# Optimization experiments

Measured on AMD Instinct MI355X. Metric: run time of the kernel, lower is better.

The kernel has to match this reference:

```python
import jax, jax.numpy as jnp
import numpy as np
import math

D = 256       # d_model
H = 8         # n_head
HD = D // H   # head dim = 32
L = 24        # n_layer
DFF = 1024    # d_ff
MAX_STEP = 512
EPS = 1e-5


def _make_pe():
    # positions repeated in groups of 3 (repeat_integers)
    pos = np.repeat(np.arange(MAX_STEP), 3).astype(np.float32)[:, None]      # [3*MAX_STEP, 1]
    div = np.exp(np.arange(0, D, 2, dtype=np.float32) * (-math.log(10000.0) / D))[None, :]
    arg = pos @ div                                                          # [3*MAX_STEP, D/2]
    pe = np.zeros((MAX_STEP * 3, D), dtype=np.float32)
    pe[:, 0::2] = np.sin(arg)
    pe[:, 1::2] = np.cos(arg)
    return jnp.asarray(pe)


def setup_inputs() -> dict:
    key = jax.random.key(0)
    ks = jax.random.split(key, 14)
    B, S = 4, 1536
    s = 0.02
    f32 = jnp.float32
    inp = {
        "x": jax.random.normal(ks[0], (B, S, D), f32),
        "pe": _make_pe(),
        "Wqkv": jax.random.normal(ks[1], (L, 3 * D, D), f32) * s,
        "bqkv": jax.random.normal(ks[2], (L, 3 * D), f32) * s,
        "Wo": jax.random.normal(ks[3], (L, D, D), f32) * s,
        "bo": jax.random.normal(ks[4], (L, D), f32) * s,
        "W1": jax.random.normal(ks[5], (L, DFF, D), f32) * s,
        "b1": jax.random.normal(ks[6], (L, DFF), f32) * s,
        "W2": jax.random.normal(ks[7], (L, D, DFF), f32) * s,
        "b2": jax.random.normal(ks[8], (L, D), f32) * s,
        "ln1_g": jnp.ones((L, D), f32),
        "ln1_b": jnp.zeros((L, D), f32),
        "ln2_g": jnp.ones((L, D), f32),
        "ln2_b": jnp.zeros((L, D), f32),
    }
    return inp


def _layernorm(y, g, b):
    m = jnp.mean(y, axis=-1, keepdims=True)
    v = jnp.mean(jnp.square(y - m), axis=-1, keepdims=True)
    return (y - m) * jax.lax.rsqrt(v + EPS) * g + b


def reference(x, pe, Wqkv, bqkv, Wo, bo, W1, b1, W2, b2, ln1_g, ln1_b, ln2_g, ln2_b):
    B, S, Dm = x.shape
    # positional embedding (positions shared within groups of 3)
    h = x + pe[None, :S]
    # block-causal mask: token i (step i//3) may attend to keys j with j//3 <= i//3
    steps = jnp.arange(S) // 3
    mask = jnp.where(steps[None, :] <= steps[:, None], 0.0, -jnp.inf)  # [S, S]
    scale = 1.0 / math.sqrt(HD)

    def layer(h, p):
        wqkv, bq, wo, bo_, w1, b1_, w2, b2_, g1, be1, g2, be2 = p
        qkv = h @ wqkv.T + bq                       # [B,S,3D]
        q, k, v = jnp.split(qkv, 3, axis=-1)
        q = q.reshape(B, S, H, HD)
        k = k.reshape(B, S, H, HD)
        v = v.reshape(B, S, H, HD)
        scores = jnp.einsum('bqhd,bkhd->bhqk', q, k) * scale + mask
        attn = jax.nn.softmax(scores, axis=-1)
        o = jnp.einsum('bhqk,bkhd->bqhd', attn, v).reshape(B, S, Dm)
        o = o @ wo.T + bo_
        h = _layernorm(h + o, g1, be1)              # post-LN
        f = jax.nn.gelu(h @ w1.T + b1_, approximate=False) @ w2.T + b2_
        h = _layernorm(h + f, g2, be2)
        return h, None

    params = (Wqkv, bqkv, Wo, bo, W1, b1, W2, b2, ln1_g, ln1_b, ln2_g, ln2_b)
    out, _ = jax.lax.scan(layer, h, params)
    return out
```

## Files before the change

kernel.cpp:

```cpp
#include <hip/hip_runtime.h>
#include <math.h>

#define SEQ   1536
#define BATCH 4
#define ROWS  (BATCH*SEQ)
#define DM    256
#define NH    8
#define HDIM  32
#define NL    24
#define DFFN  1024

typedef __bf16  bf16x4 __attribute__((ext_vector_type(4)));
typedef __bf16  bf16x8 __attribute__((ext_vector_type(8)));
typedef float   f32x4  __attribute__((ext_vector_type(4)));

__device__ __forceinline__ unsigned short f2bf(float f) {
    union { float f; unsigned int u; } v; v.f = f;
    return (unsigned short)((v.u + 0x7fffu + ((v.u >> 16) & 1u)) >> 16);
}
__device__ __forceinline__ float bf2f(unsigned short u) {
    union { unsigned int i; float f; } v; v.i = ((unsigned int)u) << 16; return v.f;
}

__device__ __forceinline__ void gload16(const void* g, void* l) {
    __builtin_amdgcn_global_load_lds(
        (const __attribute__((address_space(1))) void*)g,
        (__attribute__((address_space(3))) void*)l, 16, 0, 0);
}

__global__ __launch_bounds__(256) void w2bf_kernel(
    const float* __restrict__ src, unsigned short* __restrict__ dst)
{
    int i = (blockIdx.x * 256 + threadIdx.x) * 8;
    float4 a = *(const float4*)(src + i);
    float4 b = *(const float4*)(src + i + 4);
    union { unsigned short u[8]; uint4 v; } pk;
    pk.u[0] = f2bf(a.x); pk.u[1] = f2bf(a.y); pk.u[2] = f2bf(a.z); pk.u[3] = f2bf(a.w);
    pk.u[4] = f2bf(b.x); pk.u[5] = f2bf(b.y); pk.u[6] = f2bf(b.z); pk.u[7] = f2bf(b.w);
    *(uint4*)(dst + i) = pk.v;
}

__global__ __launch_bounds__(256) void pe_add_kernel(
    const float* __restrict__ x, const float* __restrict__ pe,
    float* __restrict__ h, unsigned short* __restrict__ hb)
{
    int i4  = blockIdx.x * 256 + threadIdx.x;
    int idx = i4 * 4;
    int row = idx >> 8;
    int d   = idx & 255;
    int s   = row % SEQ;
    float4 xv = *(const float4*)(x + idx);
    float4 pv = *(const float4*)(pe + s * DM + d);
    float4 hv;
    hv.x = xv.x + pv.x; hv.y = xv.y + pv.y; hv.z = xv.z + pv.z; hv.w = xv.w + pv.w;
    *(float4*)(h + idx) = hv;
    ushort4 hbv;
    hbv.x = f2bf(hv.x); hbv.y = f2bf(hv.y); hbv.z = f2bf(hv.z); hbv.w = f2bf(hv.w);
    *(ushort4*)(hb + idx) = hbv;
}

template<int K, int EPI>
__global__ __launch_bounds__(256) void gemm3(
    const unsigned short* __restrict__ A,
    const unsigned short* __restrict__ W,
    const float* __restrict__ bias,
    unsigned short* __restrict__ outb,
    unsigned short* __restrict__ vT)
{
    __shared__ unsigned short Ash[2][128 * 64];
    __shared__ unsigned short Bsh[2][64 * 64];
    const int m0 = blockIdx.x * 128;
    const int n0 = blockIdx.y * 64;
    const int t  = threadIdx.x;
    const int lane = t & 63;
    const int wv = t >> 6;
    const int wm = wv >> 1, wn = wv & 1;
    const int l15 = lane & 15, l4 = lane >> 4;

    const int ar = lane >> 3;
    const int sx = ((lane & 7) ^ ar) * 8;

    f32x4 acc[4][2];
    #pragma unroll
    for (int i = 0; i < 4; ++i) { acc[i][0] = (f32x4){0,0,0,0}; acc[i][1] = (f32x4){0,0,0,0}; }

    const int NT = K / 64;
    #pragma unroll
    for (int i = 0; i < 4; ++i) {
        int c = wv * 4 + i;
        gload16(&A[(size_t)(m0 + c * 8 + ar) * K + sx], &Ash[0][c * 512]);
    }
    gload16(&W[(size_t)(n0 + wv * 8 + ar) * K + sx],        &Bsh[0][wv * 512]);
    gload16(&W[(size_t)(n0 + (wv + 4) * 8 + ar) * K + sx],  &Bsh[0][(wv + 4) * 512]);
    __syncthreads();

    int cur = 0;
    for (int tt = 0; tt < NT; ++tt) {
        if (tt + 1 < NT) {
            const int k0 = (tt + 1) * 64;
            #pragma unroll
            for (int i = 0; i < 4; ++i) {
                int c = wv * 4 + i;
                gload16(&A[(size_t)(m0 + c * 8 + ar) * K + k0 + sx], &Ash[cur ^ 1][c * 512]);
            }
            gload16(&W[(size_t)(n0 + wv * 8 + ar) * K + k0 + sx],       &Bsh[cur ^ 1][wv * 512]);
            gload16(&W[(size_t)(n0 + (wv + 4) * 8 + ar) * K + k0 + sx], &Bsh[cur ^ 1][(wv + 4) * 512]);
        }
        #pragma unroll
        for (int kk = 0; kk < 2; ++kk) {
            bf16x8 af[4], bfr[2];
            #pragma unroll
            for (int mt = 0; mt < 4; ++mt) {
                int row = wm * 64 + mt * 16 + l15;
                af[mt] = *(const bf16x8*)&Ash[cur][row * 64 + (((kk * 4 + l4) ^ (l15 & 7)) * 8)];
            }
            #pragma unroll
            for (int nt = 0; nt < 2; ++nt) {
                int row = wn * 32 + nt * 16 + l15;
                bfr[nt] = *(const bf16x8*)&Bsh[cur][row * 64 + (((kk * 4 + l4) ^ (l15 & 7)) * 8)];
            }
            #pragma unroll
            for (int mt = 0; mt < 4; ++mt)
                #pragma unroll
                for (int nt = 0; nt < 2; ++nt)
                    acc[mt][nt] = __builtin_amdgcn_mfma_f32_16x16x32_bf16(af[mt], bfr[nt], acc[mt][nt], 0, 0, 0);
        }
        __syncthreads();
        cur ^= 1;
    }

    #pragma unroll
    for (int mt = 0; mt < 4; ++mt)
    #pragma unroll
    for (int nt = 0; nt < 2; ++nt)
    #pragma unroll
    for (int r = 0; r < 4; ++r) {
        int row = m0 + wm * 64 + mt * 16 + l4 * 4 + r;
        int col = n0 + wn * 32 + nt * 16 + l15;
        float val = acc[mt][nt][r] + bias[col];
        if (EPI == 0) {
            if (col < 512) {
                if (col < 256) val *= 0.17677669529663687f;
                outb[(size_t)row * 512 + col] = f2bf(val);
            } else {
                int c = col - 512; int hh = c >> 5; int d = c & 31;
                int b = row / SEQ; int s = row - b * SEQ;
                vT[(((size_t)(b * NH + hh)) * HDIM + d) * SEQ + s] = f2bf(val);
            }
        } else {
            float g = 0.5f * val * (1.0f + erff(val * 0.70710678118654752f));
            outb[(size_t)row * DFFN + col] = f2bf(g);
        }
    }
}

template<int K>
__global__ __launch_bounds__(256) void gemm_ln(
    const unsigned short* __restrict__ A,
    const unsigned short* __restrict__ W,
    const float* __restrict__ bias,
    const float* __restrict__ resid,
    const float* __restrict__ gam, const float* __restrict__ bet,
    float* __restrict__ hout, unsigned short* __restrict__ hbout)
{
    __shared__ unsigned short Ash[2][32 * 64];
    __shared__ unsigned short Bsh[2][256 * 64];
    __shared__ float red[4][32][2];
    const int m0 = blockIdx.x * 32;
    const int t  = threadIdx.x;
    const int lane = t & 63;
    const int w  = t >> 6;
    const int l15 = lane & 15, l4 = lane >> 4;
    const int ar = lane >> 3;
    const int sx = ((lane & 7) ^ ar) * 8;

    f32x4 acc[2][4];
    #pragma unroll
    for (int mt = 0; mt < 2; ++mt)
        #pragma unroll
        for (int nt = 0; nt < 4; ++nt)
            acc[mt][nt] = (f32x4){0,0,0,0};

    const int NT = K / 64;
    gload16(&A[(size_t)(m0 + w * 8 + ar) * K + sx], &Ash[0][w * 512]);
    #pragma unroll
    for (int i = 0; i < 8; ++i) {
        int c = w * 8 + i;
        gload16(&W[(size_t)(c * 8 + ar) * K + sx], &Bsh[0][c * 512]);
    }
    __syncthreads();

    int cur = 0;
    for (int tt = 0; tt < NT; ++tt) {
        if (tt + 1 < NT) {
            const int k0 = (tt + 1) * 64;
            gload16(&A[(size_t)(m0 + w * 8 + ar) * K + k0 + sx], &Ash[cur ^ 1][w * 512]);
            #pragma unroll
            for (int i = 0; i < 8; ++i) {
                int c = w * 8 + i;
                gload16(&W[(size_t)(c * 8 + ar) * K + k0 + sx], &Bsh[cur ^ 1][c * 512]);
            }
        }
        #pragma unroll
        for (int kk = 0; kk < 2; ++kk) {
            bf16x8 af[2], bfr[4];
            #pragma unroll
            for (int mt = 0; mt < 2; ++mt) {
                int row = mt * 16 + l15;
                af[mt] = *(const bf16x8*)&Ash[cur][row * 64 + (((kk * 4 + l4) ^ (l15 & 7)) * 8)];
            }
            #pragma unroll
            for (int nt = 0; nt < 4; ++nt) {
                int row = w * 64 + nt * 16 + l15;
                bfr[nt] = *(const bf16x8*)&Bsh[cur][row * 64 + (((kk * 4 + l4) ^ (l15 & 7)) * 8)];
            }
            #pragma unroll
            for (int mt = 0; mt < 2; ++mt)
                #pragma unroll
                for (int nt = 0; nt < 4; ++nt)
                    acc[mt][nt] = __builtin_amdgcn_mfma_f32_16x16x32_bf16(af[mt], bfr[nt], acc[mt][nt], 0, 0, 0);
        }
        __syncthreads();
        cur ^= 1;
    }

    float vals[2][4][4];
    float gc[4], bc[4];
    #pragma unroll
    for (int nt = 0; nt < 4; ++nt) {
        int col = w * 64 + nt * 16 + l15;
        gc[nt] = gam[col];
        bc[nt] = bet[col];
    }
    #pragma unroll
    for (int mt = 0; mt < 2; ++mt)
        #pragma unroll
        for (int r = 0; r < 4; ++r) {
            int rowl = mt * 16 + l4 * 4 + r;
            float s = 0.f, s2 = 0.f;
            #pragma unroll
            for (int nt = 0; nt < 4; ++nt) {
                int col = w * 64 + nt * 16 + l15;
                float v = acc[mt][nt][r] + bias[col]
                        + resid[(size_t)(m0 + rowl) * DM + col];
                vals[mt][nt][r] = v;
                s += v; s2 += v * v;
            }
            s  += __shfl_xor(s, 1);  s2 += __shfl_xor(s2, 1);
            s  += __shfl_xor(s, 2);  s2 += __shfl_xor(s2, 2);
            s  += __shfl_xor(s, 4);  s2 += __shfl_xor(s2, 4);
            s  += __shfl_xor(s, 8);  s2 += __shfl_xor(s2, 8);
            if (l15 == 0) { red[w][rowl][0] = s; red[w][rowl][1] = s2; }
        }
    __syncthreads();

    #pragma unroll
    for (int mt = 0; mt < 2; ++mt)
        #pragma unroll
        for (int r = 0; r < 4; ++r) {
            int rowl = mt * 16 + l4 * 4 + r;
            float tot  = red[0][rowl][0] + red[1][rowl][0] + red[2][rowl][0] + red[3][rowl][0];
            float tot2 = red[0][rowl][1] + red[1][rowl][1] + red[2][rowl][1] + red[3][rowl][1];
            float mean = tot * (1.0f / 256.0f);
            float var  = tot2 * (1.0f / 256.0f) - mean * mean;
            float rstd = rsqrtf(var + 1e-5f);
            size_t base = (size_t)(m0 + rowl) * DM;
            #pragma unroll
            for (int nt = 0; nt < 4; ++nt) {
                int col = w * 64 + nt * 16 + l15;
                float y = (vals[mt][nt][r] - mean) * rstd * gc[nt] + bc[nt];
                hout[base + col]  = y;
                hbout[base + col] = f2bf(y);
            }
        }
}

template<int K, int EPI>
__global__ __launch_bounds__(256) void gemm2f(
    const unsigned short* __restrict__ A,
    const float* __restrict__ W,
    const float* __restrict__ bias,
    float* __restrict__ outf,
    unsigned short* __restrict__ outb,
    unsigned short* __restrict__ vT,
    const float* __restrict__ resid)
{
    __shared__ unsigned short Ash[64 * 64];
    __shared__ unsigned short Bsh[64 * 64];
    const int m0 = blockIdx.x * 64;
    const int n0 = blockIdx.y * 64;
    const int t  = threadIdx.x;
    const int lane = t & 63;
    const int wv = t >> 6;
    const int wm = wv >> 1, wn = wv & 1;
    const int l15 = lane & 15, l4 = lane >> 4;
    const int ar = lane >> 3;
    const int ac = (lane & 7) * 8;
    const int c0 = wv, c1 = wv + 4;

    f32x4 acc[2][2];
    #pragma unroll
    for (int i = 0; i < 2; ++i) { acc[i][0] = (f32x4){0,0,0,0}; acc[i][1] = (f32x4){0,0,0,0}; }

    for (int k0 = 0; k0 < K; k0 += 64) {
        gload16(&A[(size_t)(m0 + c0 * 8 + ar) * K + k0 + ac], &Ash[c0 * 512]);
        gload16(&A[(size_t)(m0 + c1 * 8 + ar) * K + k0 + ac], &Ash[c1 * 512]);
        {
            int row = t >> 2, seg = (t & 3) * 16;
            const float* gw = W + (size_t)(n0 + row) * K + k0 + seg;
            float4 w0 = *(const float4*)(gw);
            float4 w1 = *(const float4*)(gw + 4);
            float4 w2 = *(const float4*)(gw + 8);
            float4 w3 = *(const float4*)(gw + 12);
            union { unsigned short u[8]; uint4 v; } p0, p1;
            p0.u[0] = f2bf(w0.x); p0.u[1] = f2bf(w0.y); p0.u[2] = f2bf(w0.z); p0.u[3] = f2bf(w0.w);
            p0.u[4] = f2bf(w1.x); p0.u[5] = f2bf(w1.y); p0.u[6] = f2bf(w1.z); p0.u[7] = f2bf(w1.w);
            p1.u[0] = f2bf(w2.x); p1.u[1] = f2bf(w2.y); p1.u[2] = f2bf(w2.z); p1.u[3] = f2bf(w2.w);
            p1.u[4] = f2bf(w3.x); p1.u[5] = f2bf(w3.y); p1.u[6] = f2bf(w3.z); p1.u[7] = f2bf(w3.w);
            *(uint4*)&Bsh[row * 64 + seg] = p0.v;
            *(uint4*)&Bsh[row * 64 + seg + 8] = p1.v;
        }
        __syncthreads();
        #pragma unroll
        for (int kk = 0; kk < 2; ++kk) {
            bf16x8 af[2], bfr[2];
            #pragma unroll
            for (int mt = 0; mt < 2; ++mt)
                af[mt] = *(const bf16x8*)&Ash[(wm * 32 + mt * 16 + l15) * 64 + kk * 32 + l4 * 8];
            #pragma unroll
            for (int nt = 0; nt < 2; ++nt)
                bfr[nt] = *(const bf16x8*)&Bsh[(wn * 32 + nt * 16 + l15) * 64 + kk * 32 + l4 * 8];
            #pragma unroll
            for (int mt = 0; mt < 2; ++mt)
                #pragma unroll
                for (int nt = 0; nt < 2; ++nt)
                    acc[mt][nt] = __builtin_amdgcn_mfma_f32_16x16x32_bf16(af[mt], bfr[nt], acc[mt][nt], 0, 0, 0);
        }
        __syncthreads();
    }

    #pragma unroll
    for (int mt = 0; mt < 2; ++mt)
    #pragma unroll
    for (int nt = 0; nt < 2; ++nt)
    #pragma unroll
    for (int r = 0; r < 4; ++r) {
        int row = m0 + wm * 32 + mt * 16 + l4 * 4 + r;
        int col = n0 + wn * 32 + nt * 16 + l15;
        float val = acc[mt][nt][r] + bias[col];
        if (EPI == 0) {
            if (col < 512) {
                if (col < 256) val *= 0.17677669529663687f;
                outb[(size_t)row * 512 + col] = f2bf(val);
            } else {
                int c = col - 512; int hh = c >> 5; int d = c & 31;
                int b = row / SEQ; int s = row - b * SEQ;
                vT[(((size_t)(b * NH + hh)) * HDIM + d) * SEQ + s] = f2bf(val);
            }
        } else if (EPI == 1) {
            outf[(size_t)row * DM + col] = val + resid[(size_t)row * DM + col];
        } else {
            float g = 0.5f * val * (1.0f + erff(val * 0.70710678118654752f));
            outb[(size_t)row * DFFN + col] = f2bf(g);
        }
    }
}

__global__ __launch_bounds__(192) void attn6(
    const unsigned short* __restrict__ qkv,
    const unsigned short* __restrict__ vT,
    unsigned short* __restrict__ ob)
{
    const int sp   = threadIdx.x >> 6;
    const int lane = threadIdx.x & 63;
    const int qt = 47 - (int)blockIdx.x;
    const int bh = blockIdx.y;
    const int b = bh >> 3, h = bh & 7;
    const int l15 = lane & 15, l4 = lane >> 4;
    const int q0 = qt * 32;

    __shared__ unsigned short P[3][2][32 * 64];
    __shared__ float sml[3][96];

    const int kend   = ((q0 + 31) / 3) * 3 + 3;
    const int ntiles = (kend + 63) >> 6;
    const int t0 = (ntiles * sp) / 3;
    const int t1 = (ntiles * (sp + 1)) / 3;
    const bool empty = (t0 >= t1);

    float* Osp = (float*)P[sp];

    if (empty) {
        #pragma unroll
        for (int i = 0; i < 16; ++i) Osp[lane + i * 64] = 0.f;
        if (lane < 32) { sml[sp][lane] = 0.f; sml[sp][32 + lane] = 0.f; }
    } else {
        const int kendc = min(t1 * 64, kend);
        const int lim_min = (q0 / 3) * 3 + 3;

        bf16x8 qf[2];
        #pragma unroll
        for (int mt = 0; mt < 2; ++mt)
            qf[mt] = *(const bf16x8*)&qkv[((size_t)(b * SEQ + q0 + mt * 16 + l15)) * 512 + h * 32 + l4 * 8];

        const int sw = (l15 & 7) << 3;
        int lim2[2];
        lim2[0] = ((q0 + l15) / 3) * 3 + 3;
        lim2[1] = ((q0 + 16 + l15) / 3) * 3 + 3;

        float lsum[2] = {0.f, 0.f};
        f32x4 of[2][2];
        const f32x4 zf = (f32x4){0.f, 0.f, 0.f, 0.f};
        of[0][0] = zf; of[0][1] = zf; of[1][0] = zf; of[1][1] = zf;

        bf16x8 kf[4];
        #pragma unroll
        for (int kt = 0; kt < 4; ++kt)
            kf[kt] = *(const bf16x8*)&qkv[((size_t)(b * SEQ + t0 * 64 + kt * 16 + l15)) * 512 + 256 + h * 32 + l4 * 8];

        int pb = 0;
        for (int j0 = t0 * 64; j0 < kendc; j0 += 64) {
            f32x4 sf[2][4];
            #pragma unroll
            for (int mt = 0; mt < 2; ++mt)
                #pragma unroll
                for (int kt = 0; kt < 4; ++kt)
                    sf[mt][kt] = __builtin_amdgcn_mfma_f32_16x16x32_bf16(kf[kt], qf[mt], zf, 0, 0, 0);

            const int jn = (j0 + 64 < kendc) ? j0 + 64 : j0;
            bf16x8 kfn[4];
            #pragma unroll
            for (int kt = 0; kt < 4; ++kt)
                kfn[kt] = *(const bf16x8*)&qkv[((size_t)(b * SEQ + jn + kt * 16 + l15)) * 512 + 256 + h * 32 + l4 * 8];
            bf16x8 vf[2][2];
            #pragma unroll
            for (int dh = 0; dh < 2; ++dh)
                #pragma unroll
                for (int ks = 0; ks < 2; ++ks)
                    vf[dh][ks] = *(const bf16x8*)&vT[(((size_t)(b * NH + h)) * HDIM + dh * 16 + l15) * SEQ + j0 + ks * 32 + l4 * 8];

            const bool masked = (j0 + 64 > lim_min);
            #pragma unroll
            for (int mt = 0; mt < 2; ++mt) {
                const int rowq = mt * 16 + l15;
                float ls = 0.f;
                #pragma unroll
                for (int kt = 0; kt < 4; ++kt) {
                    float s0 = sf[mt][kt][0], s1 = sf[mt][kt][1];
                    float s2 = sf[mt][kt][2], s3 = sf[mt][kt][3];
                    if (masked) {
                        const int kb = j0 + kt * 16 + l4 * 4;
                        const int L = lim2[mt];
                        s0 = (kb     < L) ? s0 : -INFINITY;
                        s1 = (kb + 1 < L) ? s1 : -INFINITY;
                        s2 = (kb + 2 < L) ? s2 : -INFINITY;
                        s3 = (kb + 3 < L) ? s3 : -INFINITY;
                    }
                    float p0 = __expf(s0), p1 = __expf(s1);
                    float p2 = __expf(s2), p3 = __expf(s3);
                    ls += (p0 + p1) + (p2 + p3);
                    bf16x4 pk;
                    pk[0] = (__bf16)p0; pk[1] = (__bf16)p1;
                    pk[2] = (__bf16)p2; pk[3] = (__bf16)p3;
                    *(bf16x4*)&P[sp][pb][rowq * 64 + ((kt * 16 + l4 * 4) ^ sw)] = pk;
                }
                lsum[mt] += ls;
            }

            bf16x8 pf[2][2];
            #pragma unroll
            for (int mt = 0; mt < 2; ++mt) {
                int row = mt * 16 + l15;
                #pragma unroll
                for (int ks = 0; ks < 2; ++ks)
                    pf[mt][ks] = *(const bf16x8*)&P[sp][pb][row * 64 + ((ks * 32 + l4 * 8) ^ sw)];
            }
            #pragma unroll
            for (int mt = 0; mt < 2; ++mt)
                #pragma unroll
                for (int dh = 0; dh < 2; ++dh) {
                    of[mt][dh] = __builtin_amdgcn_mfma_f32_16x16x32_bf16(pf[mt][0], vf[dh][0], of[mt][dh], 0, 0, 0);
                    of[mt][dh] = __builtin_amdgcn_mfma_f32_16x16x32_bf16(pf[mt][1], vf[dh][1], of[mt][dh], 0, 0, 0);
                }
            #pragma unroll
            for (int kt = 0; kt < 4; ++kt) kf[kt] = kfn[kt];
            pb ^= 1;
        }

        int bad = (lsum[0] > 1.0e30f || lsum[1] > 1.0e30f) ? 1 : 0;
        if (__any(bad)) {
            int lim[2][4];
            float mrow[2][4], lsumO[2][4];
            #pragma unroll
            for (int mt = 0; mt < 2; ++mt) {
                of[mt][0] = zf; of[mt][1] = zf;
                #pragma unroll
                for (int r = 0; r < 4; ++r) {
                    mrow[mt][r] = -INFINITY; lsumO[mt][r] = 0.f;
                    int q = q0 + mt * 16 + l4 * 4 + r;
                    lim[mt][r] = (q / 3) * 3 + 3;
                }
            }
            for (int j0 = t0 * 64; j0 < kendc; j0 += 64) {
                bf16x8 kfs[4];
                #pragma unroll
                for (int kt = 0; kt < 4; ++kt)
                    kfs[kt] = *(const bf16x8*)&qkv[((size_t)(b * SEQ + j0 + kt * 16 + l15)) * 512 + 256 + h * 32 + l4 * 8];
                f32x4 sf[2][4];
                #pragma unroll
                for (int mt = 0; mt < 2; ++mt)
                    #pragma unroll
                    for (int kt = 0; kt < 4; ++kt)
                        sf[mt][kt] = __builtin_amdgcn_mfma_f32_16x16x32_bf16(qf[mt], kfs[kt], zf, 0, 0, 0);
                #pragma unroll
                for (int mt = 0; mt < 2; ++mt) {
                    float alpha[4];
                    #pragma unroll
                    for (int r = 0; r < 4; ++r) {
                        const int L = lim[mt][r]; int jb = j0 + l15;
                        float s0 = (jb      < L) ? sf[mt][0][r] : -INFINITY;
                        float s1 = (jb + 16 < L) ? sf[mt][1][r] : -INFINITY;
                        float s2 = (jb + 32 < L) ? sf[mt][2][r] : -INFINITY;
                        float s3 = (jb + 48 < L) ? sf[mt][3][r] : -INFINITY;
                        float tm = fmaxf(fmaxf(s0, s1), fmaxf(s2, s3));
                        tm = fmaxf(tm, __shfl_xor(tm, 1));
                        tm = fmaxf(tm, __shfl_xor(tm, 2));
                        tm = fmaxf(tm, __shfl_xor(tm, 4));
                        tm = fmaxf(tm, __shfl_xor(tm, 8));
                        float mn = fmaxf(mrow[mt][r], tm);
                        float a  = __expf(mrow[mt][r] - mn);
                        mrow[mt][r] = mn;
                        float p0 = __expf(s0 - mn), p1 = __expf(s1 - mn);
                        float p2 = __expf(s2 - mn), p3 = __expf(s3 - mn);
                        int row = mt * 16 + l4 * 4 + r;
                        int swo = (row & 7) << 3;
                        P[sp][1][(row * 64 +      l15) ^ swo] = f2bf(p0);
                        P[sp][1][(row * 64 + 16 + l15) ^ swo] = f2bf(p1);
                        P[sp][1][(row * 64 + 32 + l15) ^ swo] = f2bf(p2);
                        P[sp][1][(row * 64 + 48 + l15) ^ swo] = f2bf(p3);
                        lsumO[mt][r] = lsumO[mt][r] * a + (p0 + p1) + (p2 + p3);
                        alpha[r] = a;
                    }
                    f32x4 av = (f32x4){alpha[0], alpha[1], alpha[2], alpha[3]};
                    of[mt][0] *= av; of[mt][1] *= av;
                }
                bf16x8 pf[2][2], vf[2][2];
                #pragma unroll
                for (int mt = 0; mt < 2; ++mt) {
                    int row = mt * 16 + l15;
                    int swo = (row & 7) << 3;
                    #pragma unroll
                    for (int ks = 0; ks < 2; ++ks)
                        pf[mt][ks] = *(const bf16x8*)&P[sp][1][(row * 64 + ks * 32 + l4 * 8) ^ swo];
                }
                #pragma unroll
                for (int dh = 0; dh < 2; ++dh)
                    #pragma unroll
                    for (int ks = 0; ks < 2; ++ks)
                        vf[dh][ks] = *(const bf16x8*)&vT[(((size_t)(b * NH + h)) * HDIM + dh * 16 + l15) * SEQ + j0 + ks * 32 + l4 * 8];
                #pragma unroll
                for (int mt = 0; mt < 2; ++mt)
                    #pragma unroll
                    for (int dh = 0; dh < 2; ++dh) {
                        of[mt][dh] = __builtin_amdgcn_mfma_f32_16x16x32_bf16(pf[mt][0], vf[dh][0], of[mt][dh], 0, 0, 0);
                        of[mt][dh] = __builtin_amdgcn_mfma_f32_16x16x32_bf16(pf[mt][1], vf[dh][1], of[mt][dh], 0, 0, 0);
                    }
            }
            #pragma unroll
            for (int mt = 0; mt < 2; ++mt)
                #pragma unroll
                for (int r = 0; r < 4; ++r) {
                    float s = lsumO[mt][r];
                    s += __shfl_xor(s, 1);
                    s += __shfl_xor(s, 2);
                    s += __shfl_xor(s, 4);
                    s += __shfl_xor(s, 8);
                    lsumO[mt][r] = s;
                }
            #pragma unroll
            for (int mt = 0; mt < 2; ++mt)
                #pragma unroll
                for (int dh = 0; dh < 2; ++dh)
                    #pragma unroll
                    for (int r = 0; r < 4; ++r)
                        Osp[(mt * 16 + l4 * 4 + r) * 32 + dh * 16 + l15] = of[mt][dh][r];
            if (l15 == 0) {
                #pragma unroll
                for (int mt = 0; mt < 2; ++mt)
                    #pragma unroll
                    for (int r = 0; r < 4; ++r) {
                        int row = mt * 16 + l4 * 4 + r;
                        sml[sp][row]      = mrow[mt][r];
                        sml[sp][32 + row] = lsumO[mt][r];
                    }
            }
        } else {
            #pragma unroll
            for (int mt = 0; mt < 2; ++mt) {
                float s = lsum[mt];
                s += __shfl_xor(s, 16);
                s += __shfl_xor(s, 32);
                lsum[mt] = s;
            }
            #pragma unroll
            for (int mt = 0; mt < 2; ++mt)
                #pragma unroll
                for (int dh = 0; dh < 2; ++dh)
                    #pragma unroll
                    for (int r = 0; r < 4; ++r)
                        Osp[(mt * 16 + l4 * 4 + r) * 32 + dh * 16 + l15] = of[mt][dh][r];
            if (lane < 32) sml[sp][lane] = 0.f;
            if (l4 == 0) {
                sml[sp][32 + l15]      = lsum[0];
                sml[sp][32 + 16 + l15] = lsum[1];
            }
        }
    }

    __syncthreads();

    const int t = threadIdx.x;
    if (t < 128) {
        const int row = t >> 2;
        const int seg = (t & 3) * 8;
        float m0 = sml[0][row], l0 = sml[0][32 + row];
        float m1 = sml[1][row], l1 = sml[1][32 + row];
        float m2 = sml[2][row], l2 = sml[2][32 + row];
        float mt = fmaxf(fmaxf(m0, m1), m2);
        float w0 = __expf(m0 - mt), w1 = __expf(m1 - mt), w2 = __expf(m2 - mt);
        float inv = 1.0f / (w0 * l0 + w1 * l1 + w2 * l2);
        const float* O0 = (const float*)P[0];
        const float* O1 = (const float*)P[1];
        const float* O2 = (const float*)P[2];
        union { unsigned short u[8]; uint4 v; } pk;
        #pragma unroll
        for (int j = 0; j < 8; ++j) {
            int idx = row * 32 + seg + j;
            pk.u[j] = f2bf((w0 * O0[idx] + w1 * O1[idx] + w2 * O2[idx]) * inv);
        }
        *(uint4*)&ob[((size_t)(b * SEQ + q0 + row)) * DM + h * 32 + seg] = pk.v;
    }
}

__global__ __launch_bounds__(256) void ln_kernel(
    const float* __restrict__ rin,
    const float* __restrict__ gam, const float* __restrict__ bet,
    float* __restrict__ hout, unsigned short* __restrict__ hbout)
{
    int wv = threadIdx.x >> 6, lane = threadIdx.x & 63;
    int row = blockIdx.x * 4 + wv;
    float4 x = *(const float4*)(rin + (size_t)row * DM + lane * 4);
    float s = x.x + x.y + x.z + x.w;
    #pragma unroll
    for (int m = 1; m < 64; m <<= 1) s += __shfl_xor(s, m);
    float mean = s * (1.0f / 256.0f);
    float d0 = x.x - mean, d1 = x.y - mean, d2 = x.z - mean, d3 = x.w - mean;
    float q = d0 * d0 + d1 * d1 + d2 * d2 + d3 * d3;
    #pragma unroll
    for (int m = 1; m < 64; m <<= 1) q += __shfl_xor(q, m);
    float rstd = rsqrtf(q * (1.0f / 256.0f) + 1e-5f);
    float4 g = *(const float4*)(gam + lane * 4);
    float4 b = *(const float4*)(bet + lane * 4);
    float4 y;
    y.x = d0 * rstd * g.x + b.x;
    y.y = d1 * rstd * g.y + b.y;
    y.z = d2 * rstd * g.z + b.z;
    y.w = d3 * rstd * g.w + b.w;
    *(float4*)(hout + (size_t)row * DM + lane * 4) = y;
    ushort4 hb4;
    hb4.x = f2bf(y.x); hb4.y = f2bf(y.y); hb4.z = f2bf(y.z); hb4.w = f2bf(y.w);
    *(ushort4*)(hbout + (size_t)row * DM + lane * 4) = hb4;
}

extern "C" void kernel_launch(void* const* d_in, const int* in_sizes, int n_in,
                              void* d_out, int out_size, void* d_ws, size_t ws_size,
                              hipStream_t stream) {
    const float* x    = (const float*)d_in[0];
    const float* pe   = (const float*)d_in[1];
    const float* Wqkv = (const float*)d_in[2];
    const float* bqkv = (const float*)d_in[3];
    const float* Wo   = (const float*)d_in[4];
    const float* bo   = (const float*)d_in[5];
    const float* W1   = (const float*)d_in[6];
    const float* b1   = (const float*)d_in[7];
    const float* W2   = (const float*)d_in[8];
    const float* b2   = (const float*)d_in[9];
    const float* ln1g = (const float*)d_in[10];
    const float* ln1b = (const float*)d_in[11];
    const float* ln2g = (const float*)d_in[12];
    const float* ln2b = (const float*)d_in[13];
    float* out = (float*)d_out;

    char* ws = (char*)d_ws;
    float*          h    = (float*)(ws + 0);
    unsigned short* hb   = (unsigned short*)(ws + 6291456);
    unsigned short* qkvb = (unsigned short*)(ws + 9437184);
    unsigned short* vT   = (unsigned short*)(ws + 15728640);
    unsigned short* ob   = (unsigned short*)(ws + 18874368);
    float*          rbuf = (float*)(ws + 22020096);
    unsigned short* f1b  = (unsigned short*)(ws + 28311552);
    unsigned short* WqkvB = (unsigned short*)(ws + 40894464);
    unsigned short* WoB   = (unsigned short*)(ws + 50331648);
    unsigned short* W1B   = (unsigned short*)(ws + 53477376);
    unsigned short* W2B   = (unsigned short*)(ws + 66060288);

    const bool bw = ws_size >= 78643200u;

    if (bw) {
        w2bf_kernel<<<2304, 256, 0, stream>>>(Wqkv, WqkvB);
        w2bf_kernel<<< 768, 256, 0, stream>>>(Wo,   WoB);
        w2bf_kernel<<<3072, 256, 0, stream>>>(W1,   W1B);
        w2bf_kernel<<<3072, 256, 0, stream>>>(W2,   W2B);
    }

    pe_add_kernel<<<1536, 256, 0, stream>>>(x, pe, h, hb);

    for (int l = 0; l < NL; ++l) {
        float* hdst = (l == NL - 1) ? out : h;
        if (bw) {
            gemm3<256, 0><<<dim3(48, 12), 256, 0, stream>>>(
                hb, WqkvB + (size_t)l * 768 * 256, bqkv + l * 768, qkvb, vT);
            attn6<<<dim3(48, 32), 192, 0, stream>>>(qkvb, vT, ob);
            gemm_ln<256><<<192, 256, 0, stream>>>(
                ob, WoB + (size_t)l * 256 * 256, bo + l * 256,
                h, ln1g + l * 256, ln1b + l * 256, h, hb);
            gemm3<256, 2><<<dim3(48, 16), 256, 0, stream>>>(
                hb, W1B + (size_t)l * 1024 * 256, b1 + l * 1024, f1b, nullptr);
            gemm_ln<1024><<<192, 256, 0, stream>>>(
                f1b, W2B + (size_t)l * 256 * 1024, b2 + l * 256,
                h, ln2g + l * 256, ln2b + l * 256, hdst, hb);
        } else {
            gemm2f<256, 0><<<dim3(96, 12), 256, 0, stream>>>(
                hb, Wqkv + (size_t)l * 768 * 256, bqkv + l * 768, nullptr, qkvb, vT, nullptr);
            attn6<<<dim3(48, 32), 192, 0, stream>>>(qkvb, vT, ob);
            gemm2f<256, 1><<<dim3(96, 4), 256, 0, stream>>>(
                ob, Wo + (size_t)l * 256 * 256, bo + l * 256, rbuf, nullptr, nullptr, h);
            ln_kernel<<<1536, 256, 0, stream>>>(rbuf, ln1g + l * 256, ln1b + l * 256, h, hb);
            gemm2f<256, 2><<<dim3(96, 16), 256, 0, stream>>>(
                hb, W1 + (size_t)l * 1024 * 256, b1 + l * 1024, nullptr, f1b, nullptr, nullptr);
            gemm2f<1024, 1><<<dim3(96, 4), 256, 0, stream>>>(
                f1b, W2 + (size_t)l * 256 * 1024, b2 + l * 256, rbuf, nullptr, nullptr, h);
            ln_kernel<<<1536, 256, 0, stream>>>(rbuf, ln2g + l * 256, ln2b + l * 256, hdst, hb);
        }
    }
}
```

Before: 2.157 ms.

## Fuse attention, output projection and first LayerNorm into one kernel

Adds a new kernel in which one 512-thread block handles a 32-query tile for all 8 heads, one wave per head. The attention output is written to shared memory in bf16, multiplied by Wo using double-buffered weight tiles, then bias, residual and LayerNorm are applied in the same block. This removes the global round-trip of the attention output and one kernel launch per layer. In exchange the grid shrinks from 1536 split-key blocks to 192 blocks, each wave walks its full key range serially, and LDS use per block is large. The safe-softmax fallback branch is also dropped from the old attention kernel, which only the non-bf16 weight path still uses.

```diff
diff --git a/kernel.cpp b/kernel.cpp
--- a/kernel.cpp
+++ b/kernel.cpp
@@ -268,6 +268,343 @@
             #pragma unroll
             for (int nt = 0; nt < 4; ++nt) {
                 int col = w * 64 + nt * 16 + l15;
+                float y = (vals[mt][nt][r] - mean) * rstd * gc[nt] + bc[nt];
+                hout[base + col]  = y;
+                hbout[base + col] = f2bf(y);
+            }
+        }
+}
+
+__global__ __launch_bounds__(512) void attn_wo_ln(
+    const unsigned short* __restrict__ qkv,
+    const unsigned short* __restrict__ vT,
+    const unsigned short* __restrict__ Wo,
+    const float* __restrict__ bo,
+    const float* __restrict__ resid,
+    const float* __restrict__ gam, const float* __restrict__ bet,
+    float* __restrict__ hout, unsigned short* __restrict__ hbout)
+{
+    __shared__ unsigned short P[8][32 * 64];
+    __shared__ unsigned short AO[32 * 256];
+    __shared__ unsigned short Wsh[2][256 * 64];
+    __shared__ float red[8][32];
+    __shared__ float red2[8][32];
+
+    const int w    = threadIdx.x >> 6;
+    const int lane = threadIdx.x & 63;
+    const int qt = 47 - (int)blockIdx.x;
+    const int b  = blockIdx.y;
+    const int h  = w;
+    const int l15 = lane & 15, l4 = lane >> 4;
+    const int q0 = qt * 32;
+
+    const int kend    = ((q0 + 31) / 3) * 3 + 3;
+    const int lim_min = (q0 / 3) * 3 + 3;
+
+    bf16x8 qf[2];
+    #pragma unroll
+    for (int mt = 0; mt < 2; ++mt)
+        qf[mt] = *(const bf16x8*)&qkv[((size_t)(b * SEQ + q0 + mt * 16 + l15)) * 512 + h * 32 + l4 * 8];
+
+    const int sw = (l15 & 7) << 3;
+    int lim2[2];
+    lim2[0] = ((q0 + l15) / 3) * 3 + 3;
+    lim2[1] = ((q0 + 16 + l15) / 3) * 3 + 3;
+
+    float lsum[2] = {0.f, 0.f};
+    f32x4 of[2][2];
+    const f32x4 zf = (f32x4){0.f, 0.f, 0.f, 0.f};
+    of[0][0] = zf; of[0][1] = zf; of[1][0] = zf; of[1][1] = zf;
+
+    bf16x8 kf[4];
+    #pragma unroll
+    for (int kt = 0; kt < 4; ++kt)
+        kf[kt] = *(const bf16x8*)&qkv[((size_t)(b * SEQ + kt * 16 + l15)) * 512 + 256 + h * 32 + l4 * 8];
+
+    for (int j0 = 0; j0 < kend; j0 += 64) {
+        f32x4 sf[2][4];
+        #pragma unroll
+        for (int mt = 0; mt < 2; ++mt)
+            #pragma unroll
+            for (int kt = 0; kt < 4; ++kt)
+                sf[mt][kt] = __builtin_amdgcn_mfma_f32_16x16x32_bf16(kf[kt], qf[mt], zf, 0, 0, 0);
+
+        const int jn = (j0 + 64 < kend) ? j0 + 64 : j0;
+        bf16x8 kfn[4];
+        #pragma unroll
+        for (int kt = 0; kt < 4; ++kt)
+            kfn[kt] = *(const bf16x8*)&qkv[((size_t)(b * SEQ + jn + kt * 16 + l15)) * 512 + 256 + h * 32 + l4 * 8];
+        bf16x8 vf[2][2];
+        #pragma unroll
+        for (int dh = 0; dh < 2; ++dh)
+            #pragma unroll
+            for (int ks = 0; ks < 2; ++ks)
+                vf[dh][ks] = *(const bf16x8*)&vT[(((size_t)(b * NH + h)) * HDIM + dh * 16 + l15) * SEQ + j0 + ks * 32 + l4 * 8];
+
+        const bool masked = (j0 + 64 > lim_min);
+        #pragma unroll
+        for (int mt = 0; mt < 2; ++mt) {
+            const int rowq = mt * 16 + l15;
+            float ls = 0.f;
+            #pragma unroll
+            for (int kt = 0; kt < 4; ++kt) {
+                float s0 = sf[mt][kt][0], s1 = sf[mt][kt][1];
+                float s2 = sf[mt][kt][2], s3 = sf[mt][kt][3];
+                if (masked) {
+                    const int kb = j0 + kt * 16 + l4 * 4;
+                    const int L = lim2[mt];
+                    s0 = (kb     < L) ? s0 : -INFINITY;
+                    s1 = (kb + 1 < L) ? s1 : -INFINITY;
+                    s2 = (kb + 2 < L) ? s2 : -INFINITY;
+                    s3 = (kb + 3 < L) ? s3 : -INFINITY;
+                }
+                float p0 = __expf(s0), p1 = __expf(s1);
+                float p2 = __expf(s2), p3 = __expf(s3);
+                ls += (p0 + p1) + (p2 + p3);
+                bf16x4 pk;
+                pk[0] = (__bf16)p0; pk[1] = (__bf16)p1;
+                pk[2] = (__bf16)p2; pk[3] = (__bf16)p3;
+                *(bf16x4*)&P[w][rowq * 64 + ((kt * 16 + l4 * 4) ^ sw)] = pk;
+            }
+            lsum[mt] += ls;
+        }
+
+        bf16x8 pf[2][2];
+        #pragma unroll
+        for (int mt = 0; mt < 2; ++mt) {
+            int row = mt * 16 + l15;
+            #pragma unroll
+            for (int ks = 0; ks < 2; ++ks)
+                pf[mt][ks] = *(const bf16x8*)&P[w][row * 64 + ((ks * 32 + l4 * 8) ^ sw)];
+        }
+        #pragma unroll
+        for (int mt = 0; mt < 2; ++mt)
+            #pragma unroll
+            for (int dh = 0; dh < 2; ++dh) {
+                of[mt][dh] = __builtin_amdgcn_mfma_f32_16x16x32_bf16(pf[mt][0], vf[dh][0], of[mt][dh], 0, 0, 0);
+                of[mt][dh] = __builtin_amdgcn_mfma_f32_16x16x32_bf16(pf[mt][1], vf[dh][1], of[mt][dh], 0, 0, 0);
+            }
+        #pragma unroll
+        for (int kt = 0; kt < 4; ++kt) kf[kt] = kfn[kt];
+    }
+
+    int bad = (lsum[0] > 1.0e30f || lsum[1] > 1.0e30f) ? 1 : 0;
+    if (__any(bad)) {
+        int lim[2][4];
+        float mrow[2][4], lsumO[2][4];
+        #pragma unroll
+        for (int mt = 0; mt < 2; ++mt) {
+            of[mt][0] = zf; of[mt][1] = zf;
+            #pragma unroll
+            for (int r = 0; r < 4; ++r) {
+                mrow[mt][r] = -INFINITY; lsumO[mt][r] = 0.f;
+                int q = q0 + mt * 16 + l4 * 4 + r;
+                lim[mt][r] = (q / 3) * 3 + 3;
+            }
+        }
+        for (int j0 = 0; j0 < kend; j0 += 64) {
+            bf16x8 kfs[4];
+            #pragma unroll
+            for (int kt = 0; kt < 4; ++kt)
+                kfs[kt] = *(const bf16x8*)&qkv[((size_t)(b * SEQ + j0 + kt * 16 + l15)) * 512 + 256 + h * 32 + l4 * 8];
+            f32x4 sf[2][4];
+            #pragma unroll
+            for (int mt = 0; mt < 2; ++mt)
+                #pragma unroll
+                for (int kt = 0; kt < 4; ++kt)
+                    sf[mt][kt] = __builtin_amdgcn_mfma_f32_16x16x32_bf16(qf[mt], kfs[kt], zf, 0, 0, 0);
+            #pragma unroll
+            for (int mt = 0; mt < 2; ++mt) {
+                float alpha[4];
+                #pragma unroll
+                for (int r = 0; r < 4; ++r) {
+                    const int L = lim[mt][r]; int jb = j0 + l15;
+                    float s0 = (jb      < L) ? sf[mt][0][r] : -INFINITY;
+                    float s1 = (jb + 16 < L) ? sf[mt][1][r] : -INFINITY;
+                    float s2 = (jb + 32 < L) ? sf[mt][2][r] : -INFINITY;
+                    float s3 = (jb + 48 < L) ? sf[mt][3][r] : -INFINITY;
+                    float tm = fmaxf(fmaxf(s0, s1), fmaxf(s2, s3));
+                    tm = fmaxf(tm, __shfl_xor(tm, 1));
+                    tm = fmaxf(tm, __shfl_xor(tm, 2));
+                    tm = fmaxf(tm, __shfl_xor(tm, 4));
+                    tm = fmaxf(tm, __shfl_xor(tm, 8));
+                    float mn = fmaxf(mrow[mt][r], tm);
+                    float a  = __expf(mrow[mt][r] - mn);
+                    mrow[mt][r] = mn;
+                    float p0 = __expf(s0 - mn), p1 = __expf(s1 - mn);
+                    float p2 = __expf(s2 - mn), p3 = __expf(s3 - mn);
+                    int row = mt * 16 + l4 * 4 + r;
+                    int swo = (row & 7) << 3;
+                    P[w][(row * 64 +      l15) ^ swo] = f2bf(p0);
+                    P[w][(row * 64 + 16 + l15) ^ swo] = f2bf(p1);
+                    P[w][(row * 64 + 32 + l15) ^ swo] = f2bf(p2);
+                    P[w][(row * 64 + 48 + l15) ^ swo] = f2bf(p3);
+                    lsumO[mt][r] = lsumO[mt][r] * a + (p0 + p1) + (p2 + p3);
+                    alpha[r] = a;
+                }
+                f32x4 av = (f32x4){alpha[0], alpha[1], alpha[2], alpha[3]};
+                of[mt][0] *= av; of[mt][1] *= av;
+            }
+            bf16x8 pf[2][2], vf[2][2];
+            #pragma unroll
+            for (int mt = 0; mt < 2; ++mt) {
+                int row = mt * 16 + l15;
+                int swo = (row & 7) << 3;
+                #pragma unroll
+                for (int ks = 0; ks < 2; ++ks)
+                    pf[mt][ks] = *(const bf16x8*)&P[w][(row * 64 + ks * 32 + l4 * 8) ^ swo];
+            }
+            #pragma unroll
+            for (int dh = 0; dh < 2; ++dh)
+                #pragma unroll
+                for (int ks = 0; ks < 2; ++ks)
+                    vf[dh][ks] = *(const bf16x8*)&vT[(((size_t)(b * NH + h)) * HDIM + dh * 16 + l15) * SEQ + j0 + ks * 32 + l4 * 8];
+            #pragma unroll
+            for (int mt = 0; mt < 2; ++mt)
+                #pragma unroll
+                for (int dh = 0; dh < 2; ++dh) {
+                    of[mt][dh] = __builtin_amdgcn_mfma_f32_16x16x32_bf16(pf[mt][0], vf[dh][0], of[mt][dh], 0, 0, 0);
+                    of[mt][dh] = __builtin_amdgcn_mfma_f32_16x16x32_bf16(pf[mt][1], vf[dh][1], of[mt][dh], 0, 0, 0);
+                }
+        }
+        #pragma unroll
+        for (int mt = 0; mt < 2; ++mt)
+            #pragma unroll
+            for (int r = 0; r < 4; ++r) {
+                float s = lsumO[mt][r];
+                s += __shfl_xor(s, 1);
+                s += __shfl_xor(s, 2);
+                s += __shfl_xor(s, 4);
+                s += __shfl_xor(s, 8);
+                lsumO[mt][r] = s;
+            }
+        #pragma unroll
+        for (int mt = 0; mt < 2; ++mt)
+            #pragma unroll
+            for (int dh = 0; dh < 2; ++dh)
+                #pragma unroll
+                for (int r = 0; r < 4; ++r) {
+                    int row = mt * 16 + l4 * 4 + r;
+                    int col = h * 32 + dh * 16 + l15;
+                    int g = (col >> 3) ^ (row & 7);
+                    AO[row * 256 + (g << 3) + (col & 7)] = f2bf(of[mt][dh][r] / lsumO[mt][r]);
+                }
+    } else {
+        #pragma unroll
+        for (int mt = 0; mt < 2; ++mt) {
+            float s = lsum[mt];
+            s += __shfl_xor(s, 16);
+            s += __shfl_xor(s, 32);
+            lsum[mt] = s;
+        }
+        #pragma unroll
+        for (int mt = 0; mt < 2; ++mt)
+            #pragma unroll
+            for (int dh = 0; dh < 2; ++dh)
+                #pragma unroll
+                for (int r = 0; r < 4; ++r) {
+                    int row = mt * 16 + l4 * 4 + r;
+                    float ls = __shfl(lsum[mt], l4 * 4 + r);
+                    int col = h * 32 + dh * 16 + l15;
+                    int g = (col >> 3) ^ (row & 7);
+                    AO[row * 256 + (g << 3) + (col & 7)] = f2bf(of[mt][dh][r] / ls);
+                }
+    }
+
+    __syncthreads();
+
+    const int ar = lane >> 3;
+    const int sx = ((lane & 7) ^ ar) * 8;
+
+    f32x4 acc[2][2];
+    acc[0][0] = zf; acc[0][1] = zf; acc[1][0] = zf; acc[1][1] = zf;
+
+    #pragma unroll
+    for (int i = 0; i < 4; ++i) {
+        int c = w * 4 + i;
+        gload16(&Wo[(size_t)(c * 8 + ar) * 256 + sx], &Wsh[0][c * 512]);
+    }
+    __syncthreads();
+
+    int cur = 0;
+    for (int tt = 0; tt < 4; ++tt) {
+        if (tt + 1 < 4) {
+            const int k0 = (tt + 1) * 64;
+            #pragma unroll
+            for (int i = 0; i < 4; ++i) {
+                int c = w * 4 + i;
+                gload16(&Wo[(size_t)(c * 8 + ar) * 256 + k0 + sx], &Wsh[cur ^ 1][c * 512]);
+            }
+        }
+        #pragma unroll
+        for (int kk = 0; kk < 2; ++kk) {
+            bf16x8 af[2], bfr[2];
+            #pragma unroll
+            for (int mt = 0; mt < 2; ++mt) {
+                int row = mt * 16 + l15;
+                int g = (tt * 8 + kk * 4 + l4) ^ (l15 & 7);
+                af[mt] = *(const bf16x8*)&AO[row * 256 + (g << 3)];
+            }
+            #pragma unroll
+            for (int nt = 0; nt < 2; ++nt) {
+                int row = w * 32 + nt * 16 + l15;
+                bfr[nt] = *(const bf16x8*)&Wsh[cur][row * 64 + (((kk * 4 + l4) ^ (l15 & 7)) * 8)];
+            }
+            #pragma unroll
+            for (int mt = 0; mt < 2; ++mt)
+                #pragma unroll
+                for (int nt = 0; nt < 2; ++nt)
+                    acc[mt][nt] = __builtin_amdgcn_mfma_f32_16x16x32_bf16(af[mt], bfr[nt], acc[mt][nt], 0, 0, 0);
+        }
+        __syncthreads();
+        cur ^= 1;
+    }
+
+    float vals[2][2][4];
+    float gc[2], bc[2];
+    #pragma unroll
+    for (int nt = 0; nt < 2; ++nt) {
+        int col = w * 32 + nt * 16 + l15;
+        gc[nt] = gam[col];
+        bc[nt] = bet[col];
+    }
+    #pragma unroll
+    for (int mt = 0; mt < 2; ++mt)
+        #pragma unroll
+        for (int r = 0; r < 4; ++r) {
+            int rowl = mt * 16 + l4 * 4 + r;
+            float s = 0.f, s2 = 0.f;
+            #pragma unroll
+            for (int nt = 0; nt < 2; ++nt) {
+                int col = w * 32 + nt * 16 + l15;
+                float v = acc[mt][nt][r] + bo[col]
+                        + resid[(size_t)(b * SEQ + q0 + rowl) * DM + col];
+                vals[mt][nt][r] = v;
+                s += v; s2 += v * v;
+            }
+            s  += __shfl_xor(s, 1);  s2 += __shfl_xor(s2, 1);
+            s  += __shfl_xor(s, 2);  s2 += __shfl_xor(s2, 2);
+            s  += __shfl_xor(s, 4);  s2 += __shfl_xor(s2, 4);
+            s  += __shfl_xor(s, 8);  s2 += __shfl_xor(s2, 8);
+            if (l15 == 0) { red[w][rowl] = s; red2[w][rowl] = s2; }
+        }
+    __syncthreads();
+
+    #pragma unroll
+    for (int mt = 0; mt < 2; ++mt)
+        #pragma unroll
+        for (int r = 0; r < 4; ++r) {
+            int rowl = mt * 16 + l4 * 4 + r;
+            float tot = 0.f, tot2 = 0.f;
+            #pragma unroll
+            for (int ww = 0; ww < 8; ++ww) { tot += red[ww][rowl]; tot2 += red2[ww][rowl]; }
+            float mean = tot * (1.0f / 256.0f);
+            float var  = tot2 * (1.0f / 256.0f) - mean * mean;
+            float rstd = rsqrtf(var + 1e-5f);
+            size_t base = (size_t)(b * SEQ + q0 + rowl) * DM;
+            #pragma unroll
+            for (int nt = 0; nt < 2; ++nt) {
+                int col = w * 32 + nt * 16 + l15;
                 float y = (vals[mt][nt][r] - mean) * rstd * gc[nt] + bc[nt];
                 hout[base + col]  = y;
                 hbout[base + col] = f2bf(y);
@@ -487,133 +824,24 @@
             pb ^= 1;
         }
 
-        int bad = (lsum[0] > 1.0e30f || lsum[1] > 1.0e30f) ? 1 : 0;
-        if (__any(bad)) {
-            int lim[2][4];
-            float mrow[2][4], lsumO[2][4];
-            #pragma unroll
-            for (int mt = 0; mt < 2; ++mt) {
-                of[mt][0] = zf; of[mt][1] = zf;
-                #pragma unroll
-                for (int r = 0; r < 4; ++r) {
-                    mrow[mt][r] = -INFINITY; lsumO[mt][r] = 0.f;
-                    int q = q0 + mt * 16 + l4 * 4 + r;
-                    lim[mt][r] = (q / 3) * 3 + 3;
-                }
-            }
-            for (int j0 = t0 * 64; j0 < kendc; j0 += 64) {
-                bf16x8 kfs[4];
-                #pragma unroll
-                for (int kt = 0; kt < 4; ++kt)
-                    kfs[kt] = *(const bf16x8*)&qkv[((size_t)(b * SEQ + j0 + kt * 16 + l15)) * 512 + 256 + h * 32 + l4 * 8];
-                f32x4 sf[2][4];
-                #pragma unroll
-                for (int mt = 0; mt < 2; ++mt)
-                    #pragma unroll
-                    for (int kt = 0; kt < 4; ++kt)
-                        sf[mt][kt] = __builtin_amdgcn_mfma_f32_16x16x32_bf16(qf[mt], kfs[kt], zf, 0, 0, 0);
-                #pragma unroll
-                for (int mt = 0; mt < 2; ++mt) {
-                    float alpha[4];
-                    #pragma unroll
-                    for (int r = 0; r < 4; ++r) {
-                        const int L = lim[mt][r]; int jb = j0 + l15;
-                        float s0 = (jb      < L) ? sf[mt][0][r] : -INFINITY;
-                        float s1 = (jb + 16 < L) ? sf[mt][1][r] : -INFINITY;
-                        float s2 = (jb + 32 < L) ? sf[mt][2][r] : -INFINITY;
-                        float s3 = (jb + 48 < L) ? sf[mt][3][r] : -INFINITY;
-                        float tm = fmaxf(fmaxf(s0, s1), fmaxf(s2, s3));
-                        tm = fmaxf(tm, __shfl_xor(tm, 1));
-                        tm = fmaxf(tm, __shfl_xor(tm, 2));
-                        tm = fmaxf(tm, __shfl_xor(tm, 4));
-                        tm = fmaxf(tm, __shfl_xor(tm, 8));
-                        float mn = fmaxf(mrow[mt][r], tm);
-                        float a  = __expf(mrow[mt][r] - mn);
-                        mrow[mt][r] = mn;
-                        float p0 = __expf(s0 - mn), p1 = __expf(s1 - mn);
-                        float p2 = __expf(s2 - mn), p3 = __expf(s3 - mn);
-                        int row = mt * 16 + l4 * 4 + r;
-                        int swo = (row & 7) << 3;
-                        P[sp][1][(row * 64 +      l15) ^ swo] = f2bf(p0);
-                        P[sp][1][(row * 64 + 16 + l15) ^ swo] = f2bf(p1);
-                        P[sp][1][(row * 64 + 32 + l15) ^ swo] = f2bf(p2);
-                        P[sp][1][(row * 64 + 48 + l15) ^ swo] = f2bf(p3);
-                        lsumO[mt][r] = lsumO[mt][r] * a + (p0 + p1) + (p2 + p3);
-                        alpha[r] = a;
-                    }
-                    f32x4 av = (f32x4){alpha[0], alpha[1], alpha[2], alpha[3]};
-                    of[mt][0] *= av; of[mt][1] *= av;
-                }
-                bf16x8 pf[2][2], vf[2][2];
-                #pragma unroll
-                for (int mt = 0; mt < 2; ++mt) {
-                    int row = mt * 16 + l15;
-                    int swo = (row & 7) << 3;
-                    #pragma unroll
-                    for (int ks = 0; ks < 2; ++ks)
-                        pf[mt][ks] = *(const bf16x8*)&P[sp][1][(row * 64 + ks * 32 + l4 * 8) ^ swo];
-                }
-                #pragma unroll
-                for (int dh = 0; dh < 2; ++dh)
-                    #pragma unroll
-                    for (int ks = 0; ks < 2; ++ks)
-                        vf[dh][ks] = *(const bf16x8*)&vT[(((size_t)(b * NH + h)) * HDIM + dh * 16 + l15) * SEQ + j0 + ks * 32 + l4 * 8];
-                #pragma unroll
-                for (int mt = 0; mt < 2; ++mt)
-                    #pragma unroll
-                    for (int dh = 0; dh < 2; ++dh) {
-                        of[mt][dh] = __builtin_amdgcn_mfma_f32_16x16x32_bf16(pf[mt][0], vf[dh][0], of[mt][dh], 0, 0, 0);
-                        of[mt][dh] = __builtin_amdgcn_mfma_f32_16x16x32_bf16(pf[mt][1], vf[dh][1], of[mt][dh], 0, 0, 0);
-                    }
-            }
-            #pragma unroll
-            for (int mt = 0; mt < 2; ++mt)
-                #pragma unroll
-                for (int r = 0; r < 4; ++r) {
-                    float s = lsumO[mt][r];
-                    s += __shfl_xor(s, 1);
-                    s += __shfl_xor(s, 2);
-                    s += __shfl_xor(s, 4);
-                    s += __shfl_xor(s, 8);
-                    lsumO[mt][r] = s;
-                }
-            #pragma unroll
-            for (int mt = 0; mt < 2; ++mt)
-                #pragma unroll
-                for (int dh = 0; dh < 2; ++dh)
-                    #pragma unroll
-                    for (int r = 0; r < 4; ++r)
-                        Osp[(mt * 16 + l4 * 4 + r) * 32 + dh * 16 + l15] = of[mt][dh][r];
-            if (l15 == 0) {
-                #pragma unroll
-                for (int mt = 0; mt < 2; ++mt)
-                    #pragma unroll
-                    for (int r = 0; r < 4; ++r) {
-                        int row = mt * 16 + l4 * 4 + r;
-                        sml[sp][row]      = mrow[mt][r];
-                        sml[sp][32 + row] = lsumO[mt][r];
-                    }
-            }
-        } else {
-            #pragma unroll
-            for (int mt = 0; mt < 2; ++mt) {
-                float s = lsum[mt];
-                s += __shfl_xor(s, 16);
-                s += __shfl_xor(s, 32);
-                lsum[mt] = s;
-            }
-            #pragma unroll
-            for (int mt = 0; mt < 2; ++mt)
-                #pragma unroll
-                for (int dh = 0; dh < 2; ++dh)
-                    #pragma unroll
-                    for (int r = 0; r < 4; ++r)
-                        Osp[(mt * 16 + l4 * 4 + r) * 32 + dh * 16 + l15] = of[mt][dh][r];
-            if (lane < 32) sml[sp][lane] = 0.f;
-            if (l4 == 0) {
-                sml[sp][32 + l15]      = lsum[0];
-                sml[sp][32 + 16 + l15] = lsum[1];
-            }
+        #pragma unroll
+        for (int mt = 0; mt < 2; ++mt) {
+            float s = lsum[mt];
+            s += __shfl_xor(s, 16);
+            s += __shfl_xor(s, 32);
+            lsum[mt] = s;
+        }
+        #pragma unroll
+        for (int mt = 0; mt < 2; ++mt)
+            #pragma unroll
+            for (int dh = 0; dh < 2; ++dh)
+                #pragma unroll
+                for (int r = 0; r < 4; ++r)
+                    Osp[(mt * 16 + l4 * 4 + r) * 32 + dh * 16 + l15] = of[mt][dh][r];
+        if (lane < 32) sml[sp][lane] = 0.f;
+        if (l4 == 0) {
+            sml[sp][32 + l15]      = lsum[0];
+            sml[sp][32 + 16 + l15] = lsum[1];
         }
     }
 
@@ -720,9 +948,8 @@
         if (bw) {
             gemm3<256, 0><<<dim3(48, 12), 256, 0, stream>>>(
                 hb, WqkvB + (size_t)l * 768 * 256, bqkv + l * 768, qkvb, vT);
-            attn6<<<dim3(48, 32), 192, 0, stream>>>(qkvb, vT, ob);
-            gemm_ln<256><<<192, 256, 0, stream>>>(
-                ob, WoB + (size_t)l * 256 * 256, bo + l * 256,
+            attn_wo_ln<<<dim3(48, 4), 512, 0, stream>>>(
+                qkvb, vT, WoB + (size_t)l * 256 * 256, bo + l * 256,
                 h, ln1g + l * 256, ln1b + l * 256, h, hb);
             gemm3<256, 2><<<dim3(48, 16), 256, 0, stream>>>(
                 hb, W1B + (size_t)l * 1024 * 256, b1 + l * 1024, f1b, nullptr);
```

New measurement: 2.390 ms. +10.8%, slower.
